# Performance work log

Measured on AMD Instinct MI355X. Metric: run time of the kernel, lower is better.

The kernel has to match this reference:

```python
import jax, jax.numpy as jnp
import numpy as np

B, T, N, D = 8, 12, 512, 64
C = 32           # number of clusters in cls_map
HID = 128
HEADS = 8
HEAD_DIM = HID // HEADS
SCALE = HEAD_DIM ** -0.5


def setup_inputs() -> dict:
    key = jax.random.key(0)
    k1, k2, k3, k4, k5 = jax.random.split(key, 5)
    x = jax.random.normal(k1, (B, T, N, D), dtype=jnp.float32)
    cls_map = jax.random.uniform(k2, (B, T, C, N), dtype=jnp.float32)
    # 1x1 Conv2d with no bias == channel-wise linear; store as [hid, in]
    s = (2.0 / D) ** 0.5
    Wq = jax.random.normal(k3, (HID, D), dtype=jnp.float32) * s
    Wk = jax.random.normal(k4, (HID, D), dtype=jnp.float32) * s
    Wv = jax.random.normal(k5, (HID, D), dtype=jnp.float32) * s
    return {"x": x, "cls_map": cls_map, "Wq": Wq, "Wk": Wk, "Wv": Wv}


def reference(x, cls_map, Wq, Wk, Wv) -> jnp.ndarray:
    Bs, Ts, Ns, _ = x.shape

    def proj(W):
        # [B,T,N,D] @ [D,HID] -> [B,T,N,HID] -> [B,T,H,N,hd]
        y = jnp.einsum('btnd,ed->btne', x, W)
        return y.reshape(Bs, Ts, Ns, HEADS, HEAD_DIM).transpose(0, 1, 3, 2, 4)

    q = proj(Wq)
    k = proj(Wk)
    v = proj(Wv)

    # scores [B,T,H,N,N]
    attn = jnp.einsum('bthnd,bthmd->bthnm', q, k) * SCALE
    attn = jax.nn.softmax(attn, axis=-1)
    # attn @ v -> [B,T,H,N,hd]; then cls pooling (cls_map broadcast over heads)
    sx = jnp.einsum('bthnm,bthmd->bthnd', attn, v)
    pooled = jnp.einsum('btcn,bthnd->bthcd', cls_map, sx)
    # [B,T,H,C,hd] -> [B,T,C,H*hd]
    out = pooled.transpose(0, 1, 3, 2, 4).reshape(Bs, Ts, cls_map.shape[2], HEADS * HEAD_DIM)
    return out
```

## Files before the change

### kernel.cpp

```cpp
#include <hip/hip_runtime.h>

constexpr int N_ = 512, D_ = 64, C_ = 32, HID_ = 128, HEADS_ = 8, HD_ = 16;
constexpr int BT_ = 96;
constexpr float LSCALE_ = 0.25f * 1.4426950408889634f;

typedef __attribute__((ext_vector_type(8))) short short8;
typedef __attribute__((ext_vector_type(4))) float f32x4;

union U8 { short8 s8; unsigned u[4]; };

static __device__ __forceinline__ unsigned short f2bf(float f) {
    unsigned u = __builtin_bit_cast(unsigned, f);
    unsigned r = (u + 0x7FFFu + ((u >> 16) & 1u)) >> 16;
    return (unsigned short)r;
}

static __device__ __forceinline__ float fexp2(float x) {
#if __has_builtin(__builtin_amdgcn_exp2f)
    return __builtin_amdgcn_exp2f(x);
#else
    return exp2f(x);
#endif
}

static __device__ __forceinline__ int vperm(int b) {
    return (b < 16) ? ((b >> 2) * 8 + (b & 3))
                    : (((b - 16) >> 2) * 8 + 4 + ((b - 16) & 3));
}

__global__ __launch_bounds__(256, 2)
void qkv_proj(const float* __restrict__ x,
              const float* __restrict__ Wq, const float* __restrict__ Wk,
              const float* __restrict__ Wv,
              unsigned short* __restrict__ qg, unsigned short* __restrict__ kg,
              unsigned short* __restrict__ vg) {
    __shared__ unsigned short xs[128 * 72];
    __shared__ unsigned short ws[384 * 72];

    const int tid = threadIdx.x;
    const int bt = blockIdx.x >> 2, rb = blockIdx.x & 3;

    for (int k = 0; k < 24; ++k) {
        const int f = tid + k * 256;
        const int m = f >> 4, c4 = f & 15;
        const float* src = (m < 128) ? Wq : (m < 256 ? Wk : Wv);
        const float4 w4 = *(const float4*)(src + (m & 127) * 64 + c4 * 4);
        const float sc = (m < 128) ? LSCALE_ : 1.0f;
        uint2 t;
        t.x = f2bf(w4.x * sc) | ((unsigned)f2bf(w4.y * sc) << 16);
        t.y = f2bf(w4.z * sc) | ((unsigned)f2bf(w4.w * sc) << 16);
        *(uint2*)(ws + m * 72 + c4 * 4) = t;
    }
    const float* xb = x + ((size_t)bt * N_ + rb * 128) * D_;
    for (int k = 0; k < 8; ++k) {
        const int f = tid + k * 256;
        const int r = f >> 4, c4 = f & 15;
        const float4 v4 = *(const float4*)(xb + r * 64 + c4 * 4);
        uint2 t;
        t.x = f2bf(v4.x) | ((unsigned)f2bf(v4.y) << 16);
        t.y = f2bf(v4.z) | ((unsigned)f2bf(v4.w) << 16);
        *(uint2*)(xs + r * 72 + c4 * 4) = t;
    }
    __syncthreads();

    const int lane = tid & 63, w = tid >> 6;
    const int g = lane >> 4, l15 = lane & 15;

    for (int nt = 0; nt < 8; ++nt) {
        const short8 b0 = *(const short8*)(xs + (nt * 16 + l15) * 72 + g * 8);
        const short8 b1 = *(const short8*)(xs + (nt * 16 + l15) * 72 + 32 + g * 8);
        for (int i = 0; i < 6; ++i) {
            const int mt = w * 6 + i;
            const unsigned short* wrow = ws + (mt * 16 + l15) * 72;
            const short8 a0 = *(const short8*)(wrow + g * 8);
            const short8 a1 = *(const short8*)(wrow + 32 + g * 8);
            f32x4 acc = {0.f, 0.f, 0.f, 0.f};
            acc = __builtin_amdgcn_mfma_f32_16x16x32_bf16(a0, b0, acc, 0, 0, 0);
            acc = __builtin_amdgcn_mfma_f32_16x16x32_bf16(a1, b1, acc, 0, 0, 0);
            const int mi = mt >> 3, h = mt & 7;
            const int nr = rb * 128 + nt * 16 + l15;
            const size_t hb = (size_t)bt * 8 + h;
            if (mi < 2) {
                unsigned short* dst = (mi == 0 ? qg : kg) + (hb * N_ + nr) * HD_ + g * 4;
                uint2 t;
                t.x = f2bf(acc[0]) | ((unsigned)f2bf(acc[1]) << 16);
                t.y = f2bf(acc[2]) | ((unsigned)f2bf(acc[3]) << 16);
                *(uint2*)dst = t;
            } else {
                unsigned short* dst = vg + hb * (N_ * HD_);
                const int nn = (nr & ~31) + vperm(nr & 31);
#pragma unroll
                for (int r = 0; r < 4; ++r)
                    dst[(g * 4 + r) * N_ + nn] = f2bf(acc[r]);
            }
        }
    }
}

__global__ __launch_bounds__(256)
void attn_pool(const unsigned short* __restrict__ qg,
               const unsigned short* __restrict__ kg,
               const unsigned short* __restrict__ vg,
               const float* __restrict__ cls_map,
               float* __restrict__ out) {
    __shared__ unsigned short k_lds[512 * 20];
    __shared__ unsigned short vt[16 * 520];
    __shared__ float den[512];

    const int tid = threadIdx.x;
    const int xcd = blockIdx.x & 7, slot = blockIdx.x >> 3;
    const int bt = xcd * 12 + (slot % 12), h = slot / 12;
    const size_t hb = (size_t)bt * 8 + h;
    const unsigned short* Kg = kg + hb * (N_ * HD_);
    const unsigned short* Vg = vg + hb * (N_ * HD_);
    const unsigned short* Qg = qg + hb * (N_ * HD_);

    for (int k = 0; k < 8; ++k) {
        const int c = tid + k * 256;
        const int row = c >> 2, q = c & 3;
        const uint2 d = *(const uint2*)(Kg + row * 16 + q * 4);
        *(uint2*)(k_lds + row * 20 + q * 4) = d;
    }
    for (int k = 0; k < 4; ++k) {
        const int c = tid + k * 256;
        const int d_ = c >> 6, col = (c & 63) * 8;
        const uint4 v4 = *(const uint4*)(Vg + d_ * 512 + col);
        *(uint4*)(vt + d_ * 520 + col) = v4;
    }

    const int lane = tid & 63, w = tid >> 6;
    const int g = lane >> 4, l15 = lane & 15;
    const int qbase = w * 128;

    short8 qf[8];
#pragma unroll
    for (int mb = 0; mb < 8; ++mb) {
        U8 f; f.u[0] = f.u[1] = f.u[2] = f.u[3] = 0u;
        if (g < 2) {
            const uint4 q4 = *(const uint4*)(Qg + (qbase + mb * 16 + l15) * 16 + g * 8);
            f.u[0] = q4.x; f.u[1] = q4.y; f.u[2] = q4.z; f.u[3] = q4.w;
        }
        qf[mb] = f.s8;
    }
    __syncthreads();

    f32x4 oacc[8];
    float dd[8];
#pragma unroll
    for (int mb = 0; mb < 8; ++mb) {
        oacc[mb] = (f32x4){0.f, 0.f, 0.f, 0.f};
        dd[mb] = 0.f;
    }
    const f32x4 zf = {0.f, 0.f, 0.f, 0.f};

    for (int j = 0; j < 16; ++j) {
        U8 ka, kb;
        ka.u[0] = ka.u[1] = ka.u[2] = ka.u[3] = 0u;
        kb.u[0] = kb.u[1] = kb.u[2] = kb.u[3] = 0u;
        if (g < 2) {
            const unsigned short* r0 = k_lds + (j * 32 + l15) * 20 + g * 8;
            const unsigned short* r1 = k_lds + (j * 32 + 16 + l15) * 20 + g * 8;
            uint2 lo = *(const uint2*)r0, hi = *(const uint2*)(r0 + 4);
            ka.u[0] = lo.x; ka.u[1] = lo.y; ka.u[2] = hi.x; ka.u[3] = hi.y;
            lo = *(const uint2*)r1; hi = *(const uint2*)(r1 + 4);
            kb.u[0] = lo.x; kb.u[1] = lo.y; kb.u[2] = hi.x; kb.u[3] = hi.y;
        }
        const short8 vf = *(const short8*)(vt + l15 * 520 + j * 32 + g * 8);

#pragma unroll
        for (int mb = 0; mb < 8; ++mb) {
            f32x4 s0 = __builtin_amdgcn_mfma_f32_16x16x32_bf16(ka.s8, qf[mb], zf, 0, 0, 0);
            f32x4 s1 = __builtin_amdgcn_mfma_f32_16x16x32_bf16(kb.s8, qf[mb], zf, 0, 0, 0);
            float e0 = fexp2(s0[0]), e1 = fexp2(s0[1]), e2 = fexp2(s0[2]), e3 = fexp2(s0[3]);
            float e4 = fexp2(s1[0]), e5 = fexp2(s1[1]), e6 = fexp2(s1[2]), e7 = fexp2(s1[3]);
            dd[mb] += ((e0 + e1) + (e2 + e3)) + ((e4 + e5) + (e6 + e7));
            U8 p;
            p.u[0] = f2bf(e0) | ((unsigned)f2bf(e1) << 16);
            p.u[1] = f2bf(e2) | ((unsigned)f2bf(e3) << 16);
            p.u[2] = f2bf(e4) | ((unsigned)f2bf(e5) << 16);
            p.u[3] = f2bf(e6) | ((unsigned)f2bf(e7) << 16);
            oacc[mb] = __builtin_amdgcn_mfma_f32_16x16x32_bf16(p.s8, vf, oacc[mb], 0, 0, 0);
        }
    }

#pragma unroll
    for (int mb = 0; mb < 8; ++mb) {
        float d = dd[mb];
        d += __shfl_xor(d, 16, 64);
        d += __shfl_xor(d, 32, 64);
        if (g == 0) den[qbase + mb * 16 + l15] = 1.0f / d;
    }
    __syncthreads();

    unsigned short* sxT = k_lds;
#pragma unroll
    for (int mb = 0; mb < 8; ++mb) {
        uint2 t;
        t.x = f2bf(oacc[mb][0]) | ((unsigned)f2bf(oacc[mb][1]) << 16);
        t.y = f2bf(oacc[mb][2]) | ((unsigned)f2bf(oacc[mb][3]) << 16);
        const int q0 = qbase + mb * 16 + g * 4;
        *(uint2*)(sxT + l15 * 520 + q0) = t;
    }
    __syncthreads();

    f32x4 pacc0 = zf, pacc1 = zf;
    const float* clsb = cls_map + (size_t)bt * C_ * N_;
    for (int kk = 0; kk < 4; ++kk) {
        const int n0 = (w * 4 + kk) * 32;
        const short8 b8 = *(const short8*)(sxT + l15 * 520 + n0 + g * 8);
        const float4 rd0 = *(const float4*)(den + n0 + g * 8);
        const float4 rd1 = *(const float4*)(den + n0 + g * 8 + 4);
        const float* c0 = clsb + l15 * N_ + n0 + g * 8;
        const float* c1 = clsb + (16 + l15) * N_ + n0 + g * 8;
        float4 ca = *(const float4*)c0, cb = *(const float4*)(c0 + 4);
        U8 a0;
        a0.u[0] = f2bf(ca.x * rd0.x) | ((unsigned)f2bf(ca.y * rd0.y) << 16);
        a0.u[1] = f2bf(ca.z * rd0.z) | ((unsigned)f2bf(ca.w * rd0.w) << 16);
        a0.u[2] = f2bf(cb.x * rd1.x) | ((unsigned)f2bf(cb.y * rd1.y) << 16);
        a0.u[3] = f2bf(cb.z * rd1.z) | ((unsigned)f2bf(cb.w * rd1.w) << 16);
        pacc0 = __builtin_amdgcn_mfma_f32_16x16x32_bf16(a0.s8, b8, pacc0, 0, 0, 0);
        ca = *(const float4*)c1; cb = *(const float4*)(c1 + 4);
        U8 a1;
        a1.u[0] = f2bf(ca.x * rd0.x) | ((unsigned)f2bf(ca.y * rd0.y) << 16);
        a1.u[1] = f2bf(ca.z * rd0.z) | ((unsigned)f2bf(ca.w * rd0.w) << 16);
        a1.u[2] = f2bf(cb.x * rd1.x) | ((unsigned)f2bf(cb.y * rd1.y) << 16);
        a1.u[3] = f2bf(cb.z * rd1.z) | ((unsigned)f2bf(cb.w * rd1.w) << 16);
        pacc1 = __builtin_amdgcn_mfma_f32_16x16x32_bf16(a1.s8, b8, pacc1, 0, 0, 0);
    }
    float* part = (float*)vt;
#pragma unroll
    for (int r = 0; r < 4; ++r) {
        part[(w * 2 + 0) * 256 + (g * 4 + r) * 16 + l15] = pacc0[r];
        part[(w * 2 + 1) * 256 + (g * 4 + r) * 16 + l15] = pacc1[r];
    }
    __syncthreads();

    float* ob = out + (size_t)bt * C_ * HID_;
    for (int o = tid; o < 512; o += 256) {
        const int c = o >> 4, dc = o & 15;
        const int mt = c >> 4, rr = c & 15;
        const int idx = mt * 256 + rr * 16 + dc;
        const float s = part[idx] + part[512 + idx] + part[1024 + idx] + part[1536 + idx];
        ob[c * HID_ + h * HD_ + dc] = s;
    }
}

extern "C" void kernel_launch(void* const* d_in, const int* in_sizes, int n_in,
                              void* d_out, int out_size, void* d_ws, size_t ws_size,
                              hipStream_t stream) {
    const float* x       = (const float*)d_in[0];
    const float* cls_map = (const float*)d_in[1];
    const float* Wq      = (const float*)d_in[2];
    const float* Wk      = (const float*)d_in[3];
    const float* Wv      = (const float*)d_in[4];
    float* out           = (float*)d_out;

    const size_t per = (size_t)BT_ * HEADS_ * N_ * HD_;
    unsigned short* qg = (unsigned short*)d_ws;
    unsigned short* kg = qg + per;
    unsigned short* vg = kg + per;

    qkv_proj<<<BT_ * 4, 256, 0, stream>>>(x, Wq, Wk, Wv, qg, kg, vg);
    attn_pool<<<BT_ * HEADS_, 256, 0, stream>>>(qg, kg, vg, cls_map, out);
}
```

Measured before the change: 137.6 us.

## Fuse QKV projection into attention kernel and use packed bf16 conversion

Drops the separate projection kernel. Each attention block now computes its own head's Q, K and V from x and writes K and V straight into LDS, with Q moved into registers through cross-lane shuffles. This removes the global bf16 Q/K/V round-trip through workspace and one kernel launch. The cost is that every (bt) row of x is re-read and re-projected by all eight head blocks, so the projection work becomes redundant. The hand-rolled bf16 rounding is also replaced with the hardware v_cvt_pk_bf16_f32 instruction.

```diff
diff --git a/kernel.cpp b/kernel.cpp
--- a/kernel.cpp
+++ b/kernel.cpp
@@ -9,10 +9,10 @@
 
 union U8 { short8 s8; unsigned u[4]; };
 
-static __device__ __forceinline__ unsigned short f2bf(float f) {
-    unsigned u = __builtin_bit_cast(unsigned, f);
-    unsigned r = (u + 0x7FFFu + ((u >> 16) & 1u)) >> 16;
-    return (unsigned short)r;
+static __device__ __forceinline__ unsigned cvtpk(float lo, float hi) {
+    unsigned r;
+    asm("v_cvt_pk_bf16_f32 %0, %1, %2" : "=v"(r) : "v"(lo), "v"(hi));
+    return r;
 }
 
 static __device__ __forceinline__ float fexp2(float x) {
@@ -28,81 +28,13 @@
                     : (((b - 16) >> 2) * 8 + 4 + ((b - 16) & 3));
 }
 
-__global__ __launch_bounds__(256, 2)
-void qkv_proj(const float* __restrict__ x,
-              const float* __restrict__ Wq, const float* __restrict__ Wk,
-              const float* __restrict__ Wv,
-              unsigned short* __restrict__ qg, unsigned short* __restrict__ kg,
-              unsigned short* __restrict__ vg) {
-    __shared__ unsigned short xs[128 * 72];
-    __shared__ unsigned short ws[384 * 72];
-
-    const int tid = threadIdx.x;
-    const int bt = blockIdx.x >> 2, rb = blockIdx.x & 3;
-
-    for (int k = 0; k < 24; ++k) {
-        const int f = tid + k * 256;
-        const int m = f >> 4, c4 = f & 15;
-        const float* src = (m < 128) ? Wq : (m < 256 ? Wk : Wv);
-        const float4 w4 = *(const float4*)(src + (m & 127) * 64 + c4 * 4);
-        const float sc = (m < 128) ? LSCALE_ : 1.0f;
-        uint2 t;
-        t.x = f2bf(w4.x * sc) | ((unsigned)f2bf(w4.y * sc) << 16);
-        t.y = f2bf(w4.z * sc) | ((unsigned)f2bf(w4.w * sc) << 16);
-        *(uint2*)(ws + m * 72 + c4 * 4) = t;
-    }
-    const float* xb = x + ((size_t)bt * N_ + rb * 128) * D_;
-    for (int k = 0; k < 8; ++k) {
-        const int f = tid + k * 256;
-        const int r = f >> 4, c4 = f & 15;
-        const float4 v4 = *(const float4*)(xb + r * 64 + c4 * 4);
-        uint2 t;
-        t.x = f2bf(v4.x) | ((unsigned)f2bf(v4.y) << 16);
-        t.y = f2bf(v4.z) | ((unsigned)f2bf(v4.w) << 16);
-        *(uint2*)(xs + r * 72 + c4 * 4) = t;
-    }
-    __syncthreads();
-
-    const int lane = tid & 63, w = tid >> 6;
-    const int g = lane >> 4, l15 = lane & 15;
-
-    for (int nt = 0; nt < 8; ++nt) {
-        const short8 b0 = *(const short8*)(xs + (nt * 16 + l15) * 72 + g * 8);
-        const short8 b1 = *(const short8*)(xs + (nt * 16 + l15) * 72 + 32 + g * 8);
-        for (int i = 0; i < 6; ++i) {
-            const int mt = w * 6 + i;
-            const unsigned short* wrow = ws + (mt * 16 + l15) * 72;
-            const short8 a0 = *(const short8*)(wrow + g * 8);
-            const short8 a1 = *(const short8*)(wrow + 32 + g * 8);
-            f32x4 acc = {0.f, 0.f, 0.f, 0.f};
-            acc = __builtin_amdgcn_mfma_f32_16x16x32_bf16(a0, b0, acc, 0, 0, 0);
-            acc = __builtin_amdgcn_mfma_f32_16x16x32_bf16(a1, b1, acc, 0, 0, 0);
-            const int mi = mt >> 3, h = mt & 7;
-            const int nr = rb * 128 + nt * 16 + l15;
-            const size_t hb = (size_t)bt * 8 + h;
-            if (mi < 2) {
-                unsigned short* dst = (mi == 0 ? qg : kg) + (hb * N_ + nr) * HD_ + g * 4;
-                uint2 t;
-                t.x = f2bf(acc[0]) | ((unsigned)f2bf(acc[1]) << 16);
-                t.y = f2bf(acc[2]) | ((unsigned)f2bf(acc[3]) << 16);
-                *(uint2*)dst = t;
-            } else {
-                unsigned short* dst = vg + hb * (N_ * HD_);
-                const int nn = (nr & ~31) + vperm(nr & 31);
-#pragma unroll
-                for (int r = 0; r < 4; ++r)
-                    dst[(g * 4 + r) * N_ + nn] = f2bf(acc[r]);
-            }
-        }
-    }
-}
-
 __global__ __launch_bounds__(256)
-void attn_pool(const unsigned short* __restrict__ qg,
-               const unsigned short* __restrict__ kg,
-               const unsigned short* __restrict__ vg,
-               const float* __restrict__ cls_map,
-               float* __restrict__ out) {
+void fused_attn(const float* __restrict__ x,
+                const float* __restrict__ cls_map,
+                const float* __restrict__ Wq, const float* __restrict__ Wk,
+                const float* __restrict__ Wv,
+                float* __restrict__ out) {
+    __shared__ unsigned short ws[48 * 72];
     __shared__ unsigned short k_lds[512 * 20];
     __shared__ unsigned short vt[16 * 520];
     __shared__ float den[512];
@@ -110,48 +42,98 @@
     const int tid = threadIdx.x;
     const int xcd = blockIdx.x & 7, slot = blockIdx.x >> 3;
     const int bt = xcd * 12 + (slot % 12), h = slot / 12;
-    const size_t hb = (size_t)bt * 8 + h;
-    const unsigned short* Kg = kg + hb * (N_ * HD_);
-    const unsigned short* Vg = vg + hb * (N_ * HD_);
-    const unsigned short* Qg = qg + hb * (N_ * HD_);
-
-    for (int k = 0; k < 8; ++k) {
-        const int c = tid + k * 256;
-        const int row = c >> 2, q = c & 3;
-        const uint2 d = *(const uint2*)(Kg + row * 16 + q * 4);
-        *(uint2*)(k_lds + row * 20 + q * 4) = d;
-    }
-    for (int k = 0; k < 4; ++k) {
-        const int c = tid + k * 256;
-        const int d_ = c >> 6, col = (c & 63) * 8;
-        const uint4 v4 = *(const uint4*)(Vg + d_ * 512 + col);
-        *(uint4*)(vt + d_ * 520 + col) = v4;
-    }
+
+    const float* __restrict__ xbt  = x + (size_t)bt * N_ * D_;
+    const float* __restrict__ clsb = cls_map + (size_t)bt * C_ * N_;
+
+    for (int k = 0; k < 3; ++k) {
+        const int f = tid + k * 256;
+        const int m = f >> 4, c4 = f & 15;
+        const float* src = (m < 16) ? (Wq + (h * 16 + m) * 64)
+                         : (m < 32) ? (Wk + (h * 16 + m - 16) * 64)
+                                    : (Wv + (h * 16 + m - 32) * 64);
+        const float4 w4 = *(const float4*)(src + c4 * 4);
+        const float sc = (m < 16) ? LSCALE_ : 1.0f;
+        uint2 t;
+        t.x = cvtpk(w4.x * sc, w4.y * sc);
+        t.y = cvtpk(w4.z * sc, w4.w * sc);
+        *(uint2*)(ws + m * 72 + c4 * 4) = t;
+    }
+    __syncthreads();
 
     const int lane = tid & 63, w = tid >> 6;
     const int g = lane >> 4, l15 = lane & 15;
     const int qbase = w * 128;
+    const f32x4 zf = {0.f, 0.f, 0.f, 0.f};
 
     short8 qf[8];
-#pragma unroll
-    for (int mb = 0; mb < 8; ++mb) {
-        U8 f; f.u[0] = f.u[1] = f.u[2] = f.u[3] = 0u;
-        if (g < 2) {
-            const uint4 q4 = *(const uint4*)(Qg + (qbase + mb * 16 + l15) * 16 + g * 8);
-            f.u[0] = q4.x; f.u[1] = q4.y; f.u[2] = q4.z; f.u[3] = q4.w;
-        }
-        qf[mb] = f.s8;
+    for (int nt = 0; nt < 8; ++nt) {
+        const int n = qbase + nt * 16 + l15;
+        const float* xr = xbt + n * 64;
+        const float4 xa = *(const float4*)(xr + g * 8);
+        const float4 xb = *(const float4*)(xr + g * 8 + 4);
+        const float4 xc = *(const float4*)(xr + 32 + g * 8);
+        const float4 xd = *(const float4*)(xr + 32 + g * 8 + 4);
+        U8 b0, b1;
+        b0.u[0] = cvtpk(xa.x, xa.y); b0.u[1] = cvtpk(xa.z, xa.w);
+        b0.u[2] = cvtpk(xb.x, xb.y); b0.u[3] = cvtpk(xb.z, xb.w);
+        b1.u[0] = cvtpk(xc.x, xc.y); b1.u[1] = cvtpk(xc.z, xc.w);
+        b1.u[2] = cvtpk(xd.x, xd.y); b1.u[3] = cvtpk(xd.z, xd.w);
+
+        {
+            const unsigned short* wr = ws + l15 * 72;
+            const short8 a0 = *(const short8*)(wr + g * 8);
+            const short8 a1 = *(const short8*)(wr + 32 + g * 8);
+            f32x4 acc = zf;
+            acc = __builtin_amdgcn_mfma_f32_16x16x32_bf16(a0, b0.s8, acc, 0, 0, 0);
+            acc = __builtin_amdgcn_mfma_f32_16x16x32_bf16(a1, b1.s8, acc, 0, 0, 0);
+            const unsigned u = cvtpk(acc[0], acc[1]), v = cvtpk(acc[2], acc[3]);
+            const int s0 = (g * 32 + l15) & 63;
+            const int s1 = (g * 32 + 16 + l15) & 63;
+            U8 q;
+            q.u[0] = (unsigned)__shfl((int)u, s0, 64);
+            q.u[1] = (unsigned)__shfl((int)v, s0, 64);
+            q.u[2] = (unsigned)__shfl((int)u, s1, 64);
+            q.u[3] = (unsigned)__shfl((int)v, s1, 64);
+            if (g >= 2) { q.u[0] = q.u[1] = q.u[2] = q.u[3] = 0u; }
+            qf[nt] = q.s8;
+        }
+        {
+            const unsigned short* wr = ws + (16 + l15) * 72;
+            const short8 a0 = *(const short8*)(wr + g * 8);
+            const short8 a1 = *(const short8*)(wr + 32 + g * 8);
+            f32x4 acc = zf;
+            acc = __builtin_amdgcn_mfma_f32_16x16x32_bf16(a0, b0.s8, acc, 0, 0, 0);
+            acc = __builtin_amdgcn_mfma_f32_16x16x32_bf16(a1, b1.s8, acc, 0, 0, 0);
+            uint2 t;
+            t.x = cvtpk(acc[0], acc[1]);
+            t.y = cvtpk(acc[2], acc[3]);
+            *(uint2*)(k_lds + n * 20 + g * 4) = t;
+        }
+        {
+            const unsigned short* wr = ws + (32 + l15) * 72;
+            const short8 a0 = *(const short8*)(wr + g * 8);
+            const short8 a1 = *(const short8*)(wr + 32 + g * 8);
+            f32x4 acc = zf;
+            acc = __builtin_amdgcn_mfma_f32_16x16x32_bf16(a0, b0.s8, acc, 0, 0, 0);
+            acc = __builtin_amdgcn_mfma_f32_16x16x32_bf16(a1, b1.s8, acc, 0, 0, 0);
+            const int blk = n >> 5;
+            const int sl = vperm(((nt & 1) << 4) + l15);
+            const unsigned u0 = cvtpk(acc[0], acc[1]);
+            const unsigned u1 = cvtpk(acc[2], acc[3]);
+            unsigned short* vr = vt + blk * 32 + sl;
+            vr[(g * 4 + 0) * 520] = (unsigned short)(u0 & 0xffffu);
+            vr[(g * 4 + 1) * 520] = (unsigned short)(u0 >> 16);
+            vr[(g * 4 + 2) * 520] = (unsigned short)(u1 & 0xffffu);
+            vr[(g * 4 + 3) * 520] = (unsigned short)(u1 >> 16);
+        }
     }
     __syncthreads();
 
     f32x4 oacc[8];
     float dd[8];
 #pragma unroll
-    for (int mb = 0; mb < 8; ++mb) {
-        oacc[mb] = (f32x4){0.f, 0.f, 0.f, 0.f};
-        dd[mb] = 0.f;
-    }
-    const f32x4 zf = {0.f, 0.f, 0.f, 0.f};
+    for (int mb = 0; mb < 8; ++mb) { oacc[mb] = zf; dd[mb] = 0.f; }
 
     for (int j = 0; j < 16; ++j) {
         U8 ka, kb;
@@ -171,14 +153,14 @@
         for (int mb = 0; mb < 8; ++mb) {
             f32x4 s0 = __builtin_amdgcn_mfma_f32_16x16x32_bf16(ka.s8, qf[mb], zf, 0, 0, 0);
             f32x4 s1 = __builtin_amdgcn_mfma_f32_16x16x32_bf16(kb.s8, qf[mb], zf, 0, 0, 0);
-            float e0 = fexp2(s0[0]), e1 = fexp2(s0[1]), e2 = fexp2(s0[2]), e3 = fexp2(s0[3]);
-            float e4 = fexp2(s1[0]), e5 = fexp2(s1[1]), e6 = fexp2(s1[2]), e7 = fexp2(s1[3]);
+            const float e0 = fexp2(s0[0]), e1 = fexp2(s0[1]), e2 = fexp2(s0[2]), e3 = fexp2(s0[3]);
+            const float e4 = fexp2(s1[0]), e5 = fexp2(s1[1]), e6 = fexp2(s1[2]), e7 = fexp2(s1[3]);
             dd[mb] += ((e0 + e1) + (e2 + e3)) + ((e4 + e5) + (e6 + e7));
             U8 p;
-            p.u[0] = f2bf(e0) | ((unsigned)f2bf(e1) << 16);
-            p.u[1] = f2bf(e2) | ((unsigned)f2bf(e3) << 16);
-            p.u[2] = f2bf(e4) | ((unsigned)f2bf(e5) << 16);
-            p.u[3] = f2bf(e6) | ((unsigned)f2bf(e7) << 16);
+            p.u[0] = cvtpk(e0, e1);
+            p.u[1] = cvtpk(e2, e3);
+            p.u[2] = cvtpk(e4, e5);
+            p.u[3] = cvtpk(e6, e7);
             oacc[mb] = __builtin_amdgcn_mfma_f32_16x16x32_bf16(p.s8, vf, oacc[mb], 0, 0, 0);
         }
     }
@@ -196,15 +178,14 @@
 #pragma unroll
     for (int mb = 0; mb < 8; ++mb) {
         uint2 t;
-        t.x = f2bf(oacc[mb][0]) | ((unsigned)f2bf(oacc[mb][1]) << 16);
-        t.y = f2bf(oacc[mb][2]) | ((unsigned)f2bf(oacc[mb][3]) << 16);
+        t.x = cvtpk(oacc[mb][0], oacc[mb][1]);
+        t.y = cvtpk(oacc[mb][2], oacc[mb][3]);
         const int q0 = qbase + mb * 16 + g * 4;
         *(uint2*)(sxT + l15 * 520 + q0) = t;
     }
     __syncthreads();
 
     f32x4 pacc0 = zf, pacc1 = zf;
-    const float* clsb = cls_map + (size_t)bt * C_ * N_;
     for (int kk = 0; kk < 4; ++kk) {
         const int n0 = (w * 4 + kk) * 32;
         const short8 b8 = *(const short8*)(sxT + l15 * 520 + n0 + g * 8);
@@ -214,17 +195,17 @@
         const float* c1 = clsb + (16 + l15) * N_ + n0 + g * 8;
         float4 ca = *(const float4*)c0, cb = *(const float4*)(c0 + 4);
         U8 a0;
-        a0.u[0] = f2bf(ca.x * rd0.x) | ((unsigned)f2bf(ca.y * rd0.y) << 16);
-        a0.u[1] = f2bf(ca.z * rd0.z) | ((unsigned)f2bf(ca.w * rd0.w) << 16);
-        a0.u[2] = f2bf(cb.x * rd1.x) | ((unsigned)f2bf(cb.y * rd1.y) << 16);
-        a0.u[3] = f2bf(cb.z * rd1.z) | ((unsigned)f2bf(cb.w * rd1.w) << 16);
+        a0.u[0] = cvtpk(ca.x * rd0.x, ca.y * rd0.y);
+        a0.u[1] = cvtpk(ca.z * rd0.z, ca.w * rd0.w);
+        a0.u[2] = cvtpk(cb.x * rd1.x, cb.y * rd1.y);
+        a0.u[3] = cvtpk(cb.z * rd1.z, cb.w * rd1.w);
         pacc0 = __builtin_amdgcn_mfma_f32_16x16x32_bf16(a0.s8, b8, pacc0, 0, 0, 0);
         ca = *(const float4*)c1; cb = *(const float4*)(c1 + 4);
         U8 a1;
-        a1.u[0] = f2bf(ca.x * rd0.x) | ((unsigned)f2bf(ca.y * rd0.y) << 16);
-        a1.u[1] = f2bf(ca.z * rd0.z) | ((unsigned)f2bf(ca.w * rd0.w) << 16);
-        a1.u[2] = f2bf(cb.x * rd1.x) | ((unsigned)f2bf(cb.y * rd1.y) << 16);
-        a1.u[3] = f2bf(cb.z * rd1.z) | ((unsigned)f2bf(cb.w * rd1.w) << 16);
+        a1.u[0] = cvtpk(ca.x * rd0.x, ca.y * rd0.y);
+        a1.u[1] = cvtpk(ca.z * rd0.z, ca.w * rd0.w);
+        a1.u[2] = cvtpk(cb.x * rd1.x, cb.y * rd1.y);
+        a1.u[3] = cvtpk(cb.z * rd1.z, cb.w * rd1.w);
         pacc1 = __builtin_amdgcn_mfma_f32_16x16x32_bf16(a1.s8, b8, pacc1, 0, 0, 0);
     }
     float* part = (float*)vt;
@@ -255,11 +236,5 @@
     const float* Wv      = (const float*)d_in[4];
     float* out           = (float*)d_out;
 
-    const size_t per = (size_t)BT_ * HEADS_ * N_ * HD_;
-    unsigned short* qg = (unsigned short*)d_ws;
-    unsigned short* kg = qg + per;
-    unsigned short* vg = kg + per;
-
-    qkv_proj<<<BT_ * 4, 256, 0, stream>>>(x, Wq, Wk, Wv, qg, kg, vg);
-    attn_pool<<<BT_ * HEADS_, 256, 0, stream>>>(qg, kg, vg, cls_map, out);
-}
+    fused_attn<<<BT_ * HEADS_, 256, 0, stream>>>(x, cls_map, Wq, Wk, Wv, out);
+}
```

Measured after the change: 151.0 us. 9.7% more time.
